# Kernel tuning notes

Measured on AMD Instinct MI355X. Metric: run time of the kernel, lower is better.

The kernel has to match this reference:

```python
import jax, jax.numpy as jnp
import numpy as np

H = 8        # num_heads
DK = 128     # head_k_dim
DV = 128     # head_v_dim
HID = 1024   # hidden_size
CHUNK = 64   # chunk size for chunked linear attention
EPS = 1e-5


def setup_inputs() -> dict:
    key = jax.random.key(0)
    ks = jax.random.split(key, 16)
    s = 0.02
    inp = {
        "hidden_states": jax.random.normal(ks[0], (2, 8192, HID), dtype=jnp.float32),
        "Wq": jax.random.normal(ks[1], (HID, HID), dtype=jnp.float32) * s,
        "Wk": jax.random.normal(ks[2], (HID, HID), dtype=jnp.float32) * s,
        "Wv": jax.random.normal(ks[3], (HID, HID), dtype=jnp.float32) * s,
        "fmq_w1": jax.random.normal(ks[4], (DK, DK), dtype=jnp.float32) * s,
        "fmq_b1": jnp.zeros((DK,), dtype=jnp.float32),
        "fmq_w2": jax.random.normal(ks[5], (DK, DK), dtype=jnp.float32) * s,
        "fmq_b2": jnp.zeros((DK,), dtype=jnp.float32),
        "fmk_w1": jax.random.normal(ks[6], (DK, DK), dtype=jnp.float32) * s,
        "fmk_b1": jnp.zeros((DK,), dtype=jnp.float32),
        "fmk_w2": jax.random.normal(ks[7], (DK, DK), dtype=jnp.float32) * s,
        "fmk_b2": jnp.zeros((DK,), dtype=jnp.float32),
        "rms_w": jnp.ones((DV,), dtype=jnp.float32),
        "Wo": jax.random.normal(ks[8], (HID, HID), dtype=jnp.float32) * s,
    }
    return inp


def reference(hidden_states, Wq, Wk, Wv, fmq_w1, fmq_b1, fmq_w2, fmq_b2,
              fmk_w1, fmk_b1, fmk_w2, fmk_b2, rms_w, Wo):
    B, T, _ = hidden_states.shape
    scale = DK ** -0.5

    # projections (torch Linear: x @ W.T), split heads -> [B,T,H,D]
    q = (hidden_states @ Wq.T).reshape(B, T, H, DK)
    k = (hidden_states @ Wk.T).reshape(B, T, H, DK)
    v = (hidden_states @ Wv.T).reshape(B, T, H, DV)

    # Hadamard feature maps: l1(x) * l2(x)
    q = (q @ fmq_w1.T + fmq_b1) * (q @ fmq_w2.T + fmq_b2)
    k = (k @ fmk_w1.T + fmk_b1) * (k @ fmk_w2.T + fmk_b2)

    q = q * scale

    # chunked causal linear attention: o_t = q_t @ sum_{s<=t} k_s v_s^T
    N = T // CHUNK
    qc = q.reshape(B, N, CHUNK, H, DK)
    kc = k.reshape(B, N, CHUNK, H, DK)
    vc = v.reshape(B, N, CHUNK, H, DV)

    # per-chunk KV outer-product sums, exclusive prefix over chunks
    kv = jnp.einsum('bnchk,bnchv->bnhkv', kc, vc)
    S = jnp.cumsum(kv, axis=1) - kv  # state entering each chunk

    o_inter = jnp.einsum('bnchk,bnhkv->bnchv', qc, S)

    # intra-chunk causal part
    A = jnp.einsum('bnihk,bnjhk->bnhij', qc, kc)
    causal = jnp.tril(jnp.ones((CHUNK, CHUNK), dtype=bool))
    A = jnp.where(causal, A, 0.0)
    o_intra = jnp.einsum('bnhij,bnjhv->bnihv', A, vc)

    o = (o_inter + o_intra).reshape(B, T, H, DV)

    # RMSNorm over head_v_dim with affine weight
    o = o * jax.lax.rsqrt(jnp.mean(o * o, axis=-1, keepdims=True) + EPS) * rms_w

    o = o.reshape(B, T, H * DV) @ Wo.T
    return o
```

## Files before the change

### kernel.cpp

```cpp
#include <hip/hip_runtime.h>

typedef __bf16 bf16x8 __attribute__((ext_vector_type(8)));
typedef float  f32x4  __attribute__((ext_vector_type(4)));

__device__ __forceinline__ float bf2f(unsigned short u) {
  union { unsigned int i; float f; } v; v.i = ((unsigned int)u) << 16; return v.f;
}
__device__ __forceinline__ unsigned short f2bf(float f) {
  union { float f; unsigned int i; } v; v.f = f;
  return (unsigned short)((v.i + 0x8000u) >> 16);
}
__device__ __forceinline__ unsigned int pk2(float a, float b) {
  union { float f; unsigned int i; } x, y; x.f = a; y.f = b;
  return ((x.i + 0x8000u) >> 16) | ((y.i + 0x8000u) & 0xFFFF0000u);
}
__device__ __forceinline__ f32x4 mfma16(bf16x8 a, bf16x8 b, f32x4 c) {
  return __builtin_amdgcn_mfma_f32_16x16x32_bf16(a, b, c, 0, 0, 0);
}
__device__ __forceinline__ void gl_lds16(const unsigned short* g, unsigned short* l) {
  __builtin_amdgcn_global_load_lds((const __attribute__((address_space(1))) void*)g,
                                   (__attribute__((address_space(3))) void*)l, 16, 0, 0);
}

__global__ void __launch_bounds__(256)
cvt_kernel(const float* __restrict__ s, unsigned short* __restrict__ d, int n4) {
  const int i = blockIdx.x * 256 + threadIdx.x;
  if (i >= n4) return;
  const float4 f = ((const float4*)s)[i];
  uint2 o; o.x = pk2(f.x, f.y); o.y = pk2(f.z, f.w);
  ((uint2*)d)[i] = o;
}
__global__ void __launch_bounds__(256)
cvt4_kernel(const float* __restrict__ s0, const float* __restrict__ s1,
            const float* __restrict__ s2, const float* __restrict__ s3,
            unsigned short* __restrict__ d0, unsigned short* __restrict__ d1,
            unsigned short* __restrict__ d2, unsigned short* __restrict__ d3,
            int n4) {
  const int w = blockIdx.y;
  const float* s = (w == 0) ? s0 : (w == 1) ? s1 : (w == 2) ? s2 : s3;
  unsigned short* d = (w == 0) ? d0 : (w == 1) ? d1 : (w == 2) ? d2 : d3;
  const int i = blockIdx.x * 256 + threadIdx.x;
  if (i >= n4) return;
  const float4 f = ((const float4*)s)[i];
  uint2 o; o.x = pk2(f.x, f.y); o.y = pk2(f.z, f.w);
  ((uint2*)d)[i] = o;
}

__device__ __forceinline__ int stage_goff(int s) {
  const int j = s >> 3, c = (s & 7) ^ (j & 7);
  return (2 * j + (c >> 2)) * 1024 + (c & 3) * 8;
}

__device__ __forceinline__ void gemm256_loop(const unsigned short* __restrict__ gA,
                                             const unsigned short* __restrict__ gB,
                                             unsigned short* __restrict__ ldsA,
                                             unsigned short* __restrict__ ldsB,
                                             int tid, f32x4 (&acc)[8][4]) {
  const int lane = tid & 63, wid = tid >> 6;
  const int lq = lane & 15, quad = lane >> 4;
  const int wm = (wid >> 2) * 128, wn = (wid & 3) * 64;

  const unsigned short* gA0 = gA + stage_goff(tid);
  const unsigned short* gA1 = gA + stage_goff(512 + tid);
  const unsigned short* gB0 = gB + stage_goff(tid);
  const unsigned short* gB1 = gB + stage_goff(512 + tid);
  const int l0 = wid * 512;
  const int l1 = 4096 + wid * 512;
  const int soff = (lq >> 1) * 64 + (((((lq & 1) << 2) + quad) ^ ((lq >> 1) & 7))) * 8;

#pragma unroll
  for (int h = 0; h < 3; ++h) {
    gl_lds16(gA0 + h * 32, ldsA + h * 8192 + l0);
    gl_lds16(gA1 + h * 32, ldsA + h * 8192 + l1);
    gl_lds16(gB0 + h * 32, ldsB + h * 8192 + l0);
    gl_lds16(gB1 + h * 32, ldsB + h * 8192 + l1);
  }
  asm volatile("s_waitcnt vmcnt(8)" ::: "memory");
  __builtin_amdgcn_s_barrier();
  __builtin_amdgcn_sched_barrier(0);

#pragma unroll
  for (int u = 0; u < 32; ++u) {
    const unsigned short* A8 = ldsA + (u & 3) * 8192;
    const unsigned short* B8 = ldsB + (u & 3) * 8192;
    unsigned short* sa = ldsA + ((u + 3) & 3) * 8192;
    unsigned short* sb = ldsB + ((u + 3) & 3) * 8192;
    bf16x8 af[4], bfr[4];
    if (u < 29) {
      gl_lds16(gA0 + (u + 3) * 32, sa + l0);
      gl_lds16(gA1 + (u + 3) * 32, sa + l1);
    }
#pragma unroll
    for (int f = 0; f < 4; ++f)
      af[f] = *(const bf16x8*)(A8 + (wm + f * 16) * 32 + soff);
#pragma unroll
    for (int g = 0; g < 4; ++g)
      bfr[g] = *(const bf16x8*)(B8 + (wn + g * 16) * 32 + soff);
    __builtin_amdgcn_s_barrier();
    __builtin_amdgcn_s_setprio(1);
#pragma unroll
    for (int f = 0; f < 4; ++f)
#pragma unroll
      for (int g = 0; g < 4; ++g) acc[f][g] = mfma16(af[f], bfr[g], acc[f][g]);
    __builtin_amdgcn_s_setprio(0);
    if (u < 29) {
      gl_lds16(gB0 + (u + 3) * 32, sb + l0);
      gl_lds16(gB1 + (u + 3) * 32, sb + l1);
    }
#pragma unroll
    for (int f = 0; f < 4; ++f)
      af[f] = *(const bf16x8*)(A8 + (wm + 64 + f * 16) * 32 + soff);
    __builtin_amdgcn_s_barrier();
    __builtin_amdgcn_s_setprio(1);
#pragma unroll
    for (int f = 0; f < 4; ++f)
#pragma unroll
      for (int g = 0; g < 4; ++g) acc[f + 4][g] = mfma16(af[f], bfr[g], acc[f + 4][g]);
    __builtin_amdgcn_s_setprio(0);
    __builtin_amdgcn_sched_barrier(0);
    if (u < 31) {
      if (u < 29)       asm volatile("s_waitcnt vmcnt(8)" ::: "memory");
      else if (u == 29) asm volatile("s_waitcnt vmcnt(4)" ::: "memory");
      else              asm volatile("s_waitcnt vmcnt(0)" ::: "memory");
      __builtin_amdgcn_s_barrier();
      __builtin_amdgcn_sched_barrier(0);
    }
  }
}

__global__ void __launch_bounds__(512, 2)
qkv_gemm256(const unsigned short* __restrict__ Xb,
            const unsigned short* __restrict__ Wqb, const unsigned short* __restrict__ Wkb,
            const unsigned short* __restrict__ Wvb,
            unsigned short* __restrict__ Q, unsigned short* __restrict__ Kf,
            unsigned short* __restrict__ VT) {
  extern __shared__ unsigned short lds[];
  const int tid = threadIdx.x;
  const int l = (blockIdx.x & 7) * 96 + (blockIdx.x >> 3);
  const int tm = l & 63, ct = l >> 6;
  const int sel = ct >> 2;
  const int rowBase = tm * 256, colBase = (ct & 3) * 256;
  const unsigned short* Bw = (sel == 0) ? Wqb : ((sel == 1) ? Wkb : Wvb);

  f32x4 acc[8][4] = {};
  gemm256_loop(Xb + (size_t)rowBase * 1024, Bw + (size_t)colBase * 1024,
               lds, lds + 32768, tid, acc);

  const int lane = tid & 63, wid = tid >> 6;
  const int lq = lane & 15, quad = lane >> 4;
  const int wm = (wid >> 2) * 128, wn = (wid & 3) * 64;
  if (sel < 2) {
    unsigned short* C = (sel == 0) ? Q : Kf;
#pragma unroll
    for (int f = 0; f < 8; ++f)
#pragma unroll
      for (int g = 0; g < 4; ++g) {
        const int col = colBase + wn + g * 16 + lq;
#pragma unroll
        for (int r = 0; r < 4; ++r) {
          const int row = rowBase + wm + f * 16 + quad * 4 + r;
          C[(size_t)row * 1024 + col] = f2bf(acc[f][g][r]);
        }
      }
  } else {
#pragma unroll
    for (int f = 0; f < 8; ++f)
#pragma unroll
      for (int g = 0; g < 4; ++g) {
        const int col = colBase + wn + g * 16 + lq;
        const int h = col >> 7, dv = col & 127;
        const int row0 = rowBase + wm + f * 16 + quad * 4;
        const int b = row0 >> 13, tl = row0 & 8191;
        ushort4 t4;
        t4.x = f2bf(acc[f][g][0]); t4.y = f2bf(acc[f][g][1]);
        t4.z = f2bf(acc[f][g][2]); t4.w = f2bf(acc[f][g][3]);
        *(ushort4*)(VT + (((size_t)(b * 8 + h) * 128 + dv) << 13) + tl) = t4;
      }
  }
}

__global__ void __launch_bounds__(512, 2)
out_gemm256(const unsigned short* __restrict__ A, const unsigned short* __restrict__ Bw,
            float* __restrict__ C) {
  extern __shared__ unsigned short lds[];
  const int tid = threadIdx.x;
  const int l = (blockIdx.x & 7) * 32 + (blockIdx.x >> 3);
  const int tm = l & 63, tn = l >> 6;
  const int rowBase = tm * 256, colBase = tn * 256;

  f32x4 acc[8][4] = {};
  gemm256_loop(A + (size_t)rowBase * 1024, Bw + (size_t)colBase * 1024,
               lds, lds + 32768, tid, acc);

  const int lane = tid & 63, wid = tid >> 6;
  const int lq = lane & 15, quad = lane >> 4;
  const int wm = (wid >> 2) * 128, wn = (wid & 3) * 64;
#pragma unroll
  for (int f = 0; f < 8; ++f)
#pragma unroll
    for (int g = 0; g < 4; ++g) {
      const int col = colBase + wn + g * 16 + lq;
#pragma unroll
      for (int r = 0; r < 4; ++r) {
        const int row = rowBase + wm + f * 16 + quad * 4 + r;
        C[(size_t)row * 1024 + col] = acc[f][g][r];
      }
    }
}

__global__ void __launch_bounds__(256)
fm_kernel(unsigned short* __restrict__ Qb, unsigned short* __restrict__ Kb,
          const unsigned short* __restrict__ fq1b, const unsigned short* __restrict__ fq2b,
          const unsigned short* __restrict__ fk1b, const unsigned short* __restrict__ fk2b,
          const float* __restrict__ fqb1, const float* __restrict__ fqb2,
          const float* __restrict__ fkb1, const float* __restrict__ fkb2) {
  __shared__ unsigned short Aq[64 * 136];
  const int z = blockIdx.z;
  unsigned short* buf = z ? Kb : Qb;
  const unsigned short* w1b = z ? fk1b : fq1b;
  const unsigned short* w2b = z ? fk2b : fq2b;
  const float* b1 = z ? fkb1 : fqb1;
  const float* b2 = z ? fkb2 : fqb2;
  const float scale = z ? 1.0f : 0.08838834764831843f;

  const int tid = threadIdx.x;
  const int t0 = blockIdx.x * 256;
  const int h = blockIdx.y, hc = h * 128;
  const int lane = tid & 63, wid = tid >> 6, lq = lane & 15, quad = lane >> 4;
  const int wn = wid * 32;

  bf16x8 w1f[4][2], w2f[4][2];
#pragma unroll
  for (int ks = 0; ks < 4; ++ks)
#pragma unroll
    for (int j = 0; j < 2; ++j) {
      const int nr = wn + j * 16 + lq;
      w1f[ks][j] = *(const bf16x8*)(w1b + nr * 128 + ks * 32 + quad * 8);
      w2f[ks][j] = *(const bf16x8*)(w2b + nr * 128 + ks * 32 + quad * 8);
    }

  const float bb1[2] = { b1[wn + lq], b1[wn + 16 + lq] };
  const float bb2[2] = { b2[wn + lq], b2[wn + 16 + lq] };

  for (int tt = 0; tt < 4; ++tt) {
    const int tb = t0 + tt * 64;
#pragma unroll
    for (int it = 0; it < 4; ++it) {
      const int p = tid + it * 256;
      const int row = p >> 4, c8 = (p & 15) * 8;
      *(uint4*)(Aq + row * 136 + c8) =
          *(const uint4*)(buf + (size_t)(tb + row) * 1024 + hc + c8);
    }
    __syncthreads();
    f32x4 a1[4][2] = {}, a2[4][2] = {};
#pragma unroll
    for (int ks = 0; ks < 4; ++ks) {
      bf16x8 af[4];
#pragma unroll
      for (int i = 0; i < 4; ++i)
        af[i] = *(const bf16x8*)(Aq + (i * 16 + lq) * 136 + ks * 32 + quad * 8);
#pragma unroll
      for (int j = 0; j < 2; ++j)
#pragma unroll
        for (int i = 0; i < 4; ++i) {
          a1[i][j] = mfma16(af[i], w1f[ks][j], a1[i][j]);
          a2[i][j] = mfma16(af[i], w2f[ks][j], a2[i][j]);
        }
    }
    __syncthreads();
#pragma unroll
    for (int j = 0; j < 2; ++j) {
      const int col = wn + j * 16 + lq;
#pragma unroll
      for (int i = 0; i < 4; ++i)
#pragma unroll
        for (int r = 0; r < 4; ++r) {
          const float v = (a1[i][j][r] + bb1[j]) * (a2[i][j][r] + bb2[j]) * scale;
          buf[(size_t)(tb + i * 16 + quad * 4 + r) * 1024 + hc + col] = f2bf(v);
        }
    }
  }
}

__global__ void __launch_bounds__(256)
kv_kernel(const unsigned short* __restrict__ Kf, const unsigned short* __restrict__ VT,
          unsigned short* __restrict__ KV) {
  __shared__ unsigned short Kt[128 * 72];
  __shared__ unsigned short Vt[128 * 72];
  const int tid = threadIdx.x;
  const int n = blockIdx.x, bh = blockIdx.y;
  const int b = bh >> 3, h = bh & 7;
  const int t0g = b * 8192 + n * 64;
  const int tl0 = n * 64;
#pragma unroll
  for (int it = 0; it < 4; ++it) {
    const int p = tid + it * 256;
    const int d = p >> 3, c8 = (p & 7) * 8;
    *(uint4*)(Vt + d * 72 + c8) =
        *(const uint4*)(VT + (((size_t)bh * 128 + d) << 13) + tl0 + c8);
    const int tok = p >> 4, c8k = (p & 15) * 8;
    const unsigned short* src = Kf + (size_t)(t0g + tok) * 1024 + h * 128 + c8k;
    ushort4 k0 = *(const ushort4*)(src);
    ushort4 k1 = *(const ushort4*)(src + 4);
    Kt[(c8k + 0) * 72 + tok] = k0.x; Kt[(c8k + 1) * 72 + tok] = k0.y;
    Kt[(c8k + 2) * 72 + tok] = k0.z; Kt[(c8k + 3) * 72 + tok] = k0.w;
    Kt[(c8k + 4) * 72 + tok] = k1.x; Kt[(c8k + 5) * 72 + tok] = k1.y;
    Kt[(c8k + 6) * 72 + tok] = k1.z; Kt[(c8k + 7) * 72 + tok] = k1.w;
  }
  __syncthreads();
  const int lane = tid & 63, wid = tid >> 6, lq = lane & 15, quad = lane >> 4;
  const int wm = (wid >> 1) * 64, wn = (wid & 1) * 64;
  f32x4 acc[4][4] = {};
#pragma unroll
  for (int ks = 0; ks < 2; ++ks) {
    bf16x8 af[4], bfr[4];
#pragma unroll
    for (int i = 0; i < 4; ++i)
      af[i] = *(const bf16x8*)(Vt + (wm + i * 16 + lq) * 72 + ks * 32 + quad * 8);
#pragma unroll
    for (int j = 0; j < 4; ++j)
      bfr[j] = *(const bf16x8*)(Kt + (wn + j * 16 + lq) * 72 + ks * 32 + quad * 8);
#pragma unroll
    for (int i = 0; i < 4; ++i)
#pragma unroll
      for (int j = 0; j < 4; ++j) acc[i][j] = mfma16(af[i], bfr[j], acc[i][j]);
  }
  const size_t base = ((size_t)bh * 128 + n) * 16384;
#pragma unroll
  for (int i = 0; i < 4; ++i)
#pragma unroll
    for (int j = 0; j < 4; ++j)
#pragma unroll
      for (int r = 0; r < 4; ++r)
        KV[base + (size_t)(wm + i * 16 + quad * 4 + r) * 128 + wn + j * 16 + lq] =
            f2bf(acc[i][j][r]);
}

__global__ void __launch_bounds__(256)
cumsum_kernel(unsigned short* __restrict__ KV) {
  const int idx = blockIdx.x * 256 + threadIdx.x;
  const int bh = idx >> 14, e = idx & 16383;
  unsigned short* p = KV + (size_t)bh * (128 * 16384) + e;
  float run = 0.f;
  for (int n = 0; n < 128; ++n) {
    const float x = bf2f(*p);
    *p = f2bf(run);
    run += x;
    p += 16384;
  }
}

__global__ void __launch_bounds__(256)
attn_kernel(const unsigned short* __restrict__ Q, const unsigned short* __restrict__ Kf,
            const unsigned short* __restrict__ VT, const unsigned short* __restrict__ S,
            const float* __restrict__ rmsw, unsigned short* __restrict__ O) {
  __shared__ uint4 smem4[3968];
  unsigned short* sm = (unsigned short*)smem4;
  unsigned short* SQ = sm;
  unsigned short* KS = sm + 8704;
  unsigned short* VTl = sm + 17920;
  unsigned short* AL = sm + 27136;
  float* OL = (float*)sm;
  float* RED = (float*)AL;
  float* SCL = RED + 256;

  const int tid = threadIdx.x;
  const int n = blockIdx.x, bh = blockIdx.y;
  const int b = bh >> 3, h = bh & 7;
  const int t0g = b * 8192 + n * 64;
  const int tl0 = n * 64;
  const int lane = tid & 63, wid = tid >> 6, lq = lane & 15, quad = lane >> 4;

#pragma unroll
  for (int it = 0; it < 4; ++it) {
    const int p = tid + it * 256;
    const int row = p >> 4, c8 = (p & 15) * 8;
    *(uint4*)(SQ + row * 136 + c8) =
        *(const uint4*)(Q + (size_t)(t0g + row) * 1024 + h * 128 + c8);
    *(uint4*)(KS + row * 136 + c8) =
        *(const uint4*)(Kf + (size_t)(t0g + row) * 1024 + h * 128 + c8);
    const int d = p >> 3, c8b = (p & 7) * 8;
    *(uint4*)(VTl + d * 72 + c8b) =
        *(const uint4*)(VT + (((size_t)bh * 128 + d) << 13) + tl0 + c8b);
  }
  __syncthreads();

  {
    f32x4 aa[4] = {};
#pragma unroll
    for (int ks = 0; ks < 4; ++ks) {
      bf16x8 kf = *(const bf16x8*)(KS + (wid * 16 + lq) * 136 + ks * 32 + quad * 8);
#pragma unroll
      for (int i = 0; i < 4; ++i) {
        bf16x8 qf = *(const bf16x8*)(SQ + (i * 16 + lq) * 136 + ks * 32 + quad * 8);
        aa[i] = mfma16(qf, kf, aa[i]);
      }
    }
#pragma unroll
    for (int i = 0; i < 4; ++i)
#pragma unroll
      for (int r = 0; r < 4; ++r) {
        const int qp = i * 16 + quad * 4 + r, kp = wid * 16 + lq;
        AL[qp * 72 + kp] = f2bf(kp <= qp ? aa[i][r] : 0.f);
      }
  }
  __syncthreads();

  const size_t sbase = ((size_t)bh * 128 + n) * 16384;
#pragma unroll
  for (int it = 0; it < 4; ++it) {
    const int p = tid + it * 256;
    const int dv = p >> 3, c8 = (p & 7) * 8;
    *(uint4*)(KS + dv * 72 + c8) = *(const uint4*)(S + sbase + (size_t)dv * 128 + c8);
  }
  __syncthreads();

  f32x4 oa[4][2] = {};
#pragma unroll
  for (int ks = 0; ks < 2; ++ks) {
    bf16x8 bv[2], sf[2];
#pragma unroll
    for (int j = 0; j < 2; ++j) {
      bv[j] = *(const bf16x8*)(VTl + (wid * 32 + j * 16 + lq) * 72 + ks * 32 + quad * 8);
      sf[j] = *(const bf16x8*)(KS + (wid * 32 + j * 16 + lq) * 72 + ks * 32 + quad * 8);
    }
#pragma unroll
    for (int i = 0; i < 4; ++i) {
      bf16x8 af = *(const bf16x8*)(AL + (i * 16 + lq) * 72 + ks * 32 + quad * 8);
      bf16x8 qf = *(const bf16x8*)(SQ + (i * 16 + lq) * 136 + ks * 32 + quad * 8);
#pragma unroll
      for (int j = 0; j < 2; ++j) {
        oa[i][j] = mfma16(af, bv[j], oa[i][j]);
        oa[i][j] = mfma16(qf, sf[j], oa[i][j]);
      }
    }
  }
  __syncthreads();

#pragma unroll
  for (int it = 0; it < 4; ++it) {
    const int p = tid + it * 256;
    const int dv = p >> 3, c8 = (p & 7) * 8;
    *(uint4*)(KS + dv * 72 + c8) =
        *(const uint4*)(S + sbase + (size_t)dv * 128 + 64 + c8);
  }
  __syncthreads();

#pragma unroll
  for (int ks = 0; ks < 2; ++ks) {
    bf16x8 sf[2];
#pragma unroll
    for (int j = 0; j < 2; ++j)
      sf[j] = *(const bf16x8*)(KS + (wid * 32 + j * 16 + lq) * 72 + ks * 32 + quad * 8);
#pragma unroll
    for (int i = 0; i < 4; ++i) {
      bf16x8 qf = *(const bf16x8*)(SQ + (i * 16 + lq) * 136 + (ks + 2) * 32 + quad * 8);
#pragma unroll
      for (int j = 0; j < 2; ++j) oa[i][j] = mfma16(qf, sf[j], oa[i][j]);
    }
  }
  __syncthreads();

#pragma unroll
  for (int i = 0; i < 4; ++i)
#pragma unroll
    for (int j = 0; j < 2; ++j)
#pragma unroll
      for (int r = 0; r < 4; ++r)
        OL[(i * 16 + quad * 4 + r) * 132 + wid * 32 + j * 16 + lq] = oa[i][j][r];
  __syncthreads();

  {
    const int r = tid >> 2, part = tid & 3;
    const float* pr = OL + r * 132 + part * 32;
    float s = 0.f;
#pragma unroll
    for (int c = 0; c < 32; ++c) { const float v = pr[c]; s += v * v; }
    RED[r * 4 + part] = s;
  }
  __syncthreads();
  if (tid < 64) {
    const float ms = (RED[tid * 4] + RED[tid * 4 + 1] + RED[tid * 4 + 2] + RED[tid * 4 + 3]) *
                     (1.f / 128.f);
    SCL[tid] = rsqrtf(ms + 1e-5f);
  }
  __syncthreads();

#pragma unroll
  for (int it = 0; it < 4; ++it) {
    const int r = (tid >> 4) + it * 16;
    const int c8 = (tid & 15) * 8;
    const float sc = SCL[r];
    unsigned short us[8];
#pragma unroll
    for (int e = 0; e < 8; ++e)
      us[e] = f2bf(OL[r * 132 + c8 + e] * sc * rmsw[c8 + e]);
    uint4 pk;
    pk.x = (unsigned int)us[0] | ((unsigned int)us[1] << 16);
    pk.y = (unsigned int)us[2] | ((unsigned int)us[3] << 16);
    pk.z = (unsigned int)us[4] | ((unsigned int)us[5] << 16);
    pk.w = (unsigned int)us[6] | ((unsigned int)us[7] << 16);
    *(uint4*)(O + (size_t)(t0g + r) * 1024 + h * 128 + c8) = pk;
  }
}

extern "C" void kernel_launch(void* const* d_in, const int* in_sizes, int n_in,
                              void* d_out, int out_size, void* d_ws, size_t ws_size,
                              hipStream_t stream) {
  const float* X    = (const float*)d_in[0];
  const float* Wq   = (const float*)d_in[1];
  const float* Wk   = (const float*)d_in[2];
  const float* Wv   = (const float*)d_in[3];
  const float* fq1  = (const float*)d_in[4];
  const float* fqb1 = (const float*)d_in[5];
  const float* fq2  = (const float*)d_in[6];
  const float* fqb2 = (const float*)d_in[7];
  const float* fk1  = (const float*)d_in[8];
  const float* fkb1 = (const float*)d_in[9];
  const float* fk2  = (const float*)d_in[10];
  const float* fkb2 = (const float*)d_in[11];
  const float* rmsw = (const float*)d_in[12];
  const float* Wo   = (const float*)d_in[13];

  static bool attr_done = false;
  if (!attr_done) {
    (void)hipFuncSetAttribute((const void*)qkv_gemm256,
                              hipFuncAttributeMaxDynamicSharedMemorySize, 131072);
    (void)hipFuncSetAttribute((const void*)out_gemm256,
                              hipFuncAttributeMaxDynamicSharedMemorySize, 131072);
    attr_done = true;
  }

  const size_t MB = 1u << 20;
  char* ws = (char*)d_ws;
  unsigned short* Q    = (unsigned short*)(ws);
  unsigned short* Kf   = (unsigned short*)(ws + 32 * MB);
  unsigned short* VT   = (unsigned short*)(ws + 64 * MB);
  unsigned short* KV   = (unsigned short*)(ws + 96 * MB);
  unsigned short* Xb   = KV;
  unsigned short* Wqb  = (unsigned short*)(ws + 160 * MB);
  unsigned short* Wkb  = (unsigned short*)(ws + 162 * MB);
  unsigned short* Wvb  = (unsigned short*)(ws + 164 * MB);
  unsigned short* Wob  = (unsigned short*)(ws + 166 * MB);
  unsigned short* fq1b = (unsigned short*)(ws + 168 * MB);
  unsigned short* fq2b = fq1b + 16384;
  unsigned short* fk1b = fq1b + 32768;
  unsigned short* fk2b = fq1b + 49152;
  unsigned short* O    = Q;

  cvt4_kernel<<<dim3(1024, 4), 256, 0, stream>>>(Wq, Wk, Wv, Wo,
                                                 Wqb, Wkb, Wvb, Wob, 262144);
  cvt4_kernel<<<dim3(16, 4), 256, 0, stream>>>(fq1, fq2, fk1, fk2,
                                               fq1b, fq2b, fk1b, fk2b, 4096);
  cvt_kernel<<<16384, 256, 0, stream>>>(X, Xb, 4194304);

  qkv_gemm256<<<dim3(768), dim3(512), 131072, stream>>>(Xb, Wqb, Wkb, Wvb, Q, Kf, VT);
  fm_kernel<<<dim3(64, 8, 2), 256, 0, stream>>>(Q, Kf, fq1b, fq2b, fk1b, fk2b,
                                                fqb1, fqb2, fkb1, fkb2);
  kv_kernel<<<dim3(128, 16), 256, 0, stream>>>(Kf, VT, KV);
  cumsum_kernel<<<1024, 256, 0, stream>>>(KV);
  attn_kernel<<<dim3(128, 16), 256, 0, stream>>>(Q, Kf, VT, KV, rmsw, O);
  out_gemm256<<<dim3(256), dim3(512), 131072, stream>>>(O, Wob, (float*)d_out);
}
```

Baseline: 439.0 us.

## Double-buffer LDS fragments in registers and remap GEMM block tile order

The shared 256x256 GEMM loop now loads all A/B fragments for the next k-step into a second register set while the current step's 32 MFMAs run. This cuts the per-iteration barriers from three to one and lets LDS reads overlap MFMA work. The cost is more vector registers (two full fragment sets), which may pressure occupancy at launch_bounds(512,2). Both GEMM kernels also get a new blockIdx-to-tile mapping that groups row tiles by XCD and column tiles by launch order, meant to improve L2 reuse.

```diff
diff --git a/kernel.cpp b/kernel.cpp
--- a/kernel.cpp
+++ b/kernel.cpp
@@ -1,4 +1,5 @@
 #include <hip/hip_runtime.h>
+
 
 typedef __bf16 bf16x8 __attribute__((ext_vector_type(8)));
 typedef float  f32x4  __attribute__((ext_vector_type(4)));
@@ -75,56 +76,52 @@
     gl_lds16(gB0 + h * 32, ldsB + h * 8192 + l0);
     gl_lds16(gB1 + h * 32, ldsB + h * 8192 + l1);
   }
-  asm volatile("s_waitcnt vmcnt(8)" ::: "memory");
+  asm volatile("s_waitcnt vmcnt(4)" ::: "memory");
   __builtin_amdgcn_s_barrier();
   __builtin_amdgcn_sched_barrier(0);
 
+  bf16x8 pa[2][8], pb[2][4];
+#pragma unroll
+  for (int f = 0; f < 8; ++f)
+    pa[0][f] = *(const bf16x8*)(ldsA + (wm + f * 16) * 32 + soff);
+#pragma unroll
+  for (int g = 0; g < 4; ++g)
+    pb[0][g] = *(const bf16x8*)(ldsB + (wn + g * 16) * 32 + soff);
+
 #pragma unroll
   for (int u = 0; u < 32; ++u) {
-    const unsigned short* A8 = ldsA + (u & 3) * 8192;
-    const unsigned short* B8 = ldsB + (u & 3) * 8192;
-    unsigned short* sa = ldsA + ((u + 3) & 3) * 8192;
-    unsigned short* sb = ldsB + ((u + 3) & 3) * 8192;
-    bf16x8 af[4], bfr[4];
+    const int cur = u & 1, nxt = cur ^ 1;
+    if (u > 0) {
+      if (u < 30) asm volatile("s_waitcnt vmcnt(4)" ::: "memory");
+      else        asm volatile("s_waitcnt vmcnt(0)" ::: "memory");
+      __builtin_amdgcn_s_barrier();
+      __builtin_amdgcn_sched_barrier(0);
+    }
     if (u < 29) {
+      unsigned short* sa = ldsA + ((u + 3) & 3) * 8192;
+      unsigned short* sb = ldsB + ((u + 3) & 3) * 8192;
       gl_lds16(gA0 + (u + 3) * 32, sa + l0);
       gl_lds16(gA1 + (u + 3) * 32, sa + l1);
-    }
-#pragma unroll
-    for (int f = 0; f < 4; ++f)
-      af[f] = *(const bf16x8*)(A8 + (wm + f * 16) * 32 + soff);
-#pragma unroll
-    for (int g = 0; g < 4; ++g)
-      bfr[g] = *(const bf16x8*)(B8 + (wn + g * 16) * 32 + soff);
-    __builtin_amdgcn_s_barrier();
-    __builtin_amdgcn_s_setprio(1);
-#pragma unroll
-    for (int f = 0; f < 4; ++f)
-#pragma unroll
-      for (int g = 0; g < 4; ++g) acc[f][g] = mfma16(af[f], bfr[g], acc[f][g]);
-    __builtin_amdgcn_s_setprio(0);
-    if (u < 29) {
       gl_lds16(gB0 + (u + 3) * 32, sb + l0);
       gl_lds16(gB1 + (u + 3) * 32, sb + l1);
     }
-#pragma unroll
-    for (int f = 0; f < 4; ++f)
-      af[f] = *(const bf16x8*)(A8 + (wm + 64 + f * 16) * 32 + soff);
-    __builtin_amdgcn_s_barrier();
+    if (u < 31) {
+      const unsigned short* An = ldsA + ((u + 1) & 3) * 8192;
+      const unsigned short* Bn = ldsB + ((u + 1) & 3) * 8192;
+#pragma unroll
+      for (int f = 0; f < 8; ++f)
+        pa[nxt][f] = *(const bf16x8*)(An + (wm + f * 16) * 32 + soff);
+#pragma unroll
+      for (int g = 0; g < 4; ++g)
+        pb[nxt][g] = *(const bf16x8*)(Bn + (wn + g * 16) * 32 + soff);
+    }
     __builtin_amdgcn_s_setprio(1);
 #pragma unroll
-    for (int f = 0; f < 4; ++f)
-#pragma unroll
-      for (int g = 0; g < 4; ++g) acc[f + 4][g] = mfma16(af[f], bfr[g], acc[f + 4][g]);
+    for (int f = 0; f < 8; ++f)
+#pragma unroll
+      for (int g = 0; g < 4; ++g)
+        acc[f][g] = mfma16(pa[cur][f], pb[cur][g], acc[f][g]);
     __builtin_amdgcn_s_setprio(0);
-    __builtin_amdgcn_sched_barrier(0);
-    if (u < 31) {
-      if (u < 29)       asm volatile("s_waitcnt vmcnt(8)" ::: "memory");
-      else if (u == 29) asm volatile("s_waitcnt vmcnt(4)" ::: "memory");
-      else              asm volatile("s_waitcnt vmcnt(0)" ::: "memory");
-      __builtin_amdgcn_s_barrier();
-      __builtin_amdgcn_sched_barrier(0);
-    }
   }
 }
 
@@ -136,8 +133,9 @@
             unsigned short* __restrict__ VT) {
   extern __shared__ unsigned short lds[];
   const int tid = threadIdx.x;
-  const int l = (blockIdx.x & 7) * 96 + (blockIdx.x >> 3);
-  const int tm = l & 63, ct = l >> 6;
+  const int bx = blockIdx.x;
+  const int tm = (bx & 7) * 8 + ((bx >> 3) & 7);
+  const int ct = bx >> 6;
   const int sel = ct >> 2;
   const int rowBase = tm * 256, colBase = (ct & 3) * 256;
   const unsigned short* Bw = (sel == 0) ? Wqb : ((sel == 1) ? Wkb : Wvb);
@@ -184,8 +182,9 @@
             float* __restrict__ C) {
   extern __shared__ unsigned short lds[];
   const int tid = threadIdx.x;
-  const int l = (blockIdx.x & 7) * 32 + (blockIdx.x >> 3);
-  const int tm = l & 63, tn = l >> 6;
+  const int bx = blockIdx.x;
+  const int tm = (bx & 7) * 8 + ((bx >> 3) & 7);
+  const int tn = bx >> 6;
   const int rowBase = tm * 256, colBase = tn * 256;
 
   f32x4 acc[8][4] = {};
```

Measured after the change: 411.1 us. 1.07x faster.
